# Optimization experiments

Measured on AMD Instinct MI355X. Metric: run time of the kernel, lower is better.

Reference implementation:

```python
import jax, jax.numpy as jnp
import numpy as np

NUM_HEADS = 4
BN_EPS = 1e-5


def setup_inputs() -> dict:
    key = jax.random.key(0)
    k1, k2, k3 = jax.random.split(key, 3)
    B, C, H, W = 4, 512, 64, 64
    c_attn = 256
    x = jax.random.normal(k1, (B, C, H, W), dtype=jnp.float32)
    # 1x1 convs are plain channel matmuls: weight[out, in]
    w_qkv = jax.random.normal(k2, (3 * c_attn, c_attn), dtype=jnp.float32) * (c_attn ** -0.5)
    w_proj = jax.random.normal(k3, (c_attn, c_attn), dtype=jnp.float32) * (c_attn ** -0.5)
    gamma = jnp.ones((c_attn,), dtype=jnp.float32)
    beta = jnp.zeros((c_attn,), dtype=jnp.float32)
    return {"x": x, "w_qkv": w_qkv, "w_proj": w_proj, "gamma": gamma, "beta": beta}


def reference(x, w_qkv, w_proj, gamma, beta):
    B, C, H, W = x.shape
    c_attn = w_proj.shape[0]
    head_dim = c_attn // NUM_HEADS
    scale = head_dim ** -0.5
    N = H * W

    x_attn = x[:, :c_attn].reshape(B, c_attn, N)   # [B, c_attn, N]
    x_skip = x[:, c_attn:]                          # [B, c_skip, H, W]

    # 1x1 conv qkv (no bias): [B, 3*c_attn, N]
    qkv = jnp.einsum('oc,bcn->bon', w_qkv, x_attn)
    qkv = qkv.reshape(B, 3, NUM_HEADS, head_dim, N)
    q, k, v = qkv[:, 0], qkv[:, 1], qkv[:, 2]       # each [B, h, d, N]

    # attn[b,h,i,j] = sum_d q[b,h,d,i] * k[b,h,d,j] * scale
    attn = jnp.einsum('bhdn,bhdm->bhnm', q, k) * scale
    attn = jax.nn.softmax(attn, axis=-1)

    # out[b,h,d,i] = sum_j attn[b,h,i,j] * v[b,h,d,j]
    out = jnp.einsum('bhnm,bhdm->bhdn', attn, v).reshape(B, c_attn, N)

    # 1x1 conv proj (no bias)
    out = jnp.einsum('oc,bcn->bon', w_proj, out)

    # BatchNorm2d (training mode: batch statistics over B and spatial dims)
    mean = out.mean(axis=(0, 2), keepdims=True)
    var = out.var(axis=(0, 2), keepdims=True)  # biased variance, as torch BN
    out = (out - mean) * jax.lax.rsqrt(var + BN_EPS)
    out = out * gamma[None, :, None] + beta[None, :, None]

    out = out.reshape(B, c_attn, H, W)
    return jnp.concatenate([out, x_skip], axis=1)
```

## Files before the change

kernel.cpp:

```cpp
#include <hip/hip_runtime.h>
#include <stdint.h>

typedef float          f32x4  __attribute__((ext_vector_type(4)));
typedef __bf16         bf16x8 __attribute__((ext_vector_type(8)));
typedef unsigned short u16x4  __attribute__((ext_vector_type(4)));
typedef unsigned short u16x8  __attribute__((ext_vector_type(8)));

__device__ __forceinline__ float bf2f(unsigned short u) {
    union { uint32_t i; float f; } v; v.i = ((uint32_t)u) << 16; return v.f;
}
__device__ __forceinline__ unsigned short bfc(float f) {
    return __builtin_bit_cast(unsigned short, (__bf16)f);
}
__device__ __forceinline__ f32x4 mfma16(bf16x8 a, bf16x8 b, f32x4 c) {
    return __builtin_amdgcn_mfma_f32_16x16x32_bf16(a, b, c, 0, 0, 0);
}
__device__ __forceinline__ void async16(const unsigned short* g, unsigned short* l) {
    __builtin_amdgcn_global_load_lds(
        (const __attribute__((address_space(1))) void*)g,
        (__attribute__((address_space(3))) void*)l, 16, 0, 0);
}

#define QSC 0.18033688f

__global__ __launch_bounds__(256) void qkv_gemm(
    const float* __restrict__ x, const float* __restrict__ wqkv,
    unsigned short* __restrict__ Qb, unsigned short* __restrict__ Kb,
    unsigned short* __restrict__ Vb) {
    const int mt = blockIdx.x;
    const int nt = blockIdx.y;
    const int b  = blockIdx.z;
    const int o0 = mt * 128, n0 = nt * 128;
    __shared__ __align__(16) unsigned short Wt[128 * 72];
    __shared__ __align__(16) unsigned short Xt[128 * 72];
    const int t = threadIdx.x;
    const int lane = t & 63, w = t >> 6;
    const int wr = w >> 1, wc = w & 1;
    const int l15 = lane & 15, g = lane >> 4;

    f32x4 acc[4][4];
    const f32x4 zero = {0.f, 0.f, 0.f, 0.f};
    for (int i = 0; i < 4; i++) for (int j = 0; j < 4; j++) acc[i][j] = zero;

    for (int k0 = 0; k0 < 256; k0 += 64) {
        {
            const int row = t >> 3, col = (t & 7) * 8;
            #pragma unroll
            for (int r = 0; r < 4; r++) {
                const float* p = wqkv + (size_t)(o0 + row + r * 32) * 256 + k0 + col;
                f32x4 v0 = *(const f32x4*)p;
                f32x4 v1 = *(const f32x4*)(p + 4);
                u16x8 o8 = { bfc(v0[0]), bfc(v0[1]), bfc(v0[2]), bfc(v0[3]),
                             bfc(v1[0]), bfc(v1[1]), bfc(v1[2]), bfc(v1[3]) };
                *(u16x8*)(&Wt[(row + r * 32) * 72 + col]) = o8;
            }
        }
        {
            const int cl = t >> 4, nl = (t & 15) * 8;
            #pragma unroll
            for (int r = 0; r < 4; r++) {
                const int c = k0 + cl + r * 16;
                const float* p = x + (size_t)(b * 512 + c) * 4096 + n0 + nl;
                f32x4 v0 = *(const f32x4*)p;
                f32x4 v1 = *(const f32x4*)(p + 4);
                #pragma unroll
                for (int j = 0; j < 4; j++) Xt[(nl + j) * 72 + cl + r * 16] = bfc(v0[j]);
                #pragma unroll
                for (int j = 0; j < 4; j++) Xt[(nl + 4 + j) * 72 + cl + r * 16] = bfc(v1[j]);
            }
        }
        __syncthreads();
        #pragma unroll
        for (int kk = 0; kk < 2; kk++) {
            bf16x8 af[4], bfr[4];
            #pragma unroll
            for (int i = 0; i < 4; i++)
                af[i] = *(const bf16x8*)(&Wt[(wr * 64 + i * 16 + l15) * 72 + kk * 32 + g * 8]);
            #pragma unroll
            for (int j = 0; j < 4; j++)
                bfr[j] = *(const bf16x8*)(&Xt[(wc * 64 + j * 16 + l15) * 72 + kk * 32 + g * 8]);
            #pragma unroll
            for (int i = 0; i < 4; i++)
                #pragma unroll
                for (int j = 0; j < 4; j++)
                    acc[i][j] = mfma16(af[i], bfr[j], acc[i][j]);
        }
        __syncthreads();
    }

    #pragma unroll
    for (int i = 0; i < 4; i++) {
        const int o = o0 + wr * 64 + i * 16 + g * 4;
        #pragma unroll
        for (int j = 0; j < 4; j++) {
            const int n = n0 + wc * 64 + j * 16 + l15;
            f32x4 a = acc[i][j];
            if (o < 256) {
                u16x4 pv = { bfc(a[0] * QSC), bfc(a[1] * QSC), bfc(a[2] * QSC), bfc(a[3] * QSC) };
                const int h = o >> 6, d = o & 63;
                *(u16x4*)(&Qb[(((size_t)(b * 4 + h)) * 4096 + n) * 64 + d]) = pv;
            } else if (o < 512) {
                u16x4 pv = { bfc(a[0]), bfc(a[1]), bfc(a[2]), bfc(a[3]) };
                const int oo = o - 256; const int h = oo >> 6, d = oo & 63;
                *(u16x4*)(&Kb[(((size_t)(b * 4 + h)) * 4096 + n) * 64 + d]) = pv;
            } else {
                const int oo = o - 512; const int h = oo >> 6, d = oo & 63;
                const size_t base = (((size_t)(b * 4 + h)) * 64 + d) * 4096 + n;
                Vb[base] = bfc(a[0]); Vb[base + 4096] = bfc(a[1]);
                Vb[base + 8192] = bfc(a[2]); Vb[base + 12288] = bfc(a[3]);
            }
        }
    }
}

__global__ __launch_bounds__(256, 4) void flash_attn(
    const unsigned short* __restrict__ Qb, const unsigned short* __restrict__ Kb,
    const unsigned short* __restrict__ Vb, unsigned short* __restrict__ Opart,
    float* __restrict__ ml) {
    __shared__ __align__(16) unsigned short Kt[2][64 * 64];
    __shared__ __align__(16) unsigned short Vt[2][64 * 64];

    const int flat = (blockIdx.z * 16 + blockIdx.y) * 32 + blockIdx.x;
    const int nf = (flat & 7) * 128 + (flat >> 3);
    const int z  = nf >> 9;
    const int bh = (nf >> 5) & 15;
    const int nb = nf & 31;

    const int t = threadIdx.x, lane = t & 63, w = t >> 6;
    const int l15 = lane & 15, g = lane >> 4;
    const int xo = (l15 & 7) << 3;
    const int c0 = (g * 8) ^ xo, c1 = c0 ^ 32;
    const int vq = ((((g >> 1) ^ (l15 & 7)) << 3) | ((g & 1) << 2));

    const int rb = lane >> 3;
    const int cbe = ((lane & 7) ^ rb) << 3;
    const unsigned short* kgp = Kb + ((size_t)bh * 4096 + z * 2048 + w * 8 + rb) * 64 + cbe;
    const unsigned short* vgp = Vb + ((size_t)(bh * 64 + w * 8 + rb)) * 4096 + z * 2048 + cbe;

    auto stage = [&](int buf) {
        async16(kgp,          &Kt[buf][w * 512]);
        async16(kgp + 2048,   &Kt[buf][w * 512 + 2048]);
        async16(vgp,          &Vt[buf][w * 512]);
        async16(vgp + 131072, &Vt[buf][w * 512 + 2048]);
        kgp += 4096; vgp += 64;
    };

    bf16x8 qf[2][2];
    #pragma unroll
    for (int ntl = 0; ntl < 2; ++ntl) {
        const int nq = nb * 128 + w * 32 + ntl * 16 + l15;
        const unsigned short* qp = Qb + ((size_t)bh * 4096 + nq) * 64;
        qf[ntl][0] = *(const bf16x8*)(qp + g * 8);
        qf[ntl][1] = *(const bf16x8*)(qp + 32 + g * 8);
    }

    const bf16x8 ones8 = __builtin_bit_cast(bf16x8,
        (u16x8){0x3F80, 0x3F80, 0x3F80, 0x3F80, 0x3F80, 0x3F80, 0x3F80, 0x3F80});

    f32x4 of[4][2];
    f32x4 lf[2];
    const f32x4 zero = {0.f, 0.f, 0.f, 0.f};
    #pragma unroll
    for (int dt = 0; dt < 4; ++dt) { of[dt][0] = zero; of[dt][1] = zero; }
    lf[0] = zero; lf[1] = zero;

    stage(0);
    __syncthreads();

    for (int itp = 0; itp < 16; ++itp) {
        #pragma unroll
        for (int cur = 0; cur < 2; ++cur) {
            if (itp * 2 + cur < 31) stage(cur ^ 1);

            f32x4 st[4][2];
            __builtin_amdgcn_s_setprio(1);
            #pragma unroll
            for (int mt = 0; mt < 4; ++mt) {
                const int kro = (mt * 16 + l15) * 64;
                bf16x8 ka0 = *(const bf16x8*)(&Kt[cur][kro + c0]);
                bf16x8 ka1 = *(const bf16x8*)(&Kt[cur][kro + c1]);
                st[mt][0] = mfma16(ka1, qf[0][1], mfma16(ka0, qf[0][0], zero));
                st[mt][1] = mfma16(ka1, qf[1][1], mfma16(ka0, qf[1][0], zero));
            }
            __builtin_amdgcn_s_setprio(0);

            bf16x8 pb[2][2];
            #pragma unroll
            for (int ntl = 0; ntl < 2; ++ntl) {
                u16x4 q[4];
                #pragma unroll
                for (int mt = 0; mt < 4; ++mt) {
                    q[mt] = (u16x4){
                        bfc(__builtin_amdgcn_exp2f(st[mt][ntl][0])),
                        bfc(__builtin_amdgcn_exp2f(st[mt][ntl][1])),
                        bfc(__builtin_amdgcn_exp2f(st[mt][ntl][2])),
                        bfc(__builtin_amdgcn_exp2f(st[mt][ntl][3])) };
                }
                pb[ntl][0] = __builtin_bit_cast(bf16x8,
                    __builtin_shufflevector(q[0], q[1], 0, 1, 2, 3, 4, 5, 6, 7));
                pb[ntl][1] = __builtin_bit_cast(bf16x8,
                    __builtin_shufflevector(q[2], q[3], 0, 1, 2, 3, 4, 5, 6, 7));
            }

            const unsigned short* vb = &Vt[cur][l15 * 64];
            __builtin_amdgcn_s_setprio(1);
            lf[0] = mfma16(ones8, pb[0][1], mfma16(ones8, pb[0][0], lf[0]));
            lf[1] = mfma16(ones8, pb[1][1], mfma16(ones8, pb[1][0], lf[1]));
            #pragma unroll
            for (int dt = 0; dt < 4; ++dt) {
                const unsigned short* vr = vb + dt * 1024;
                u16x4 w00 = *(const u16x4*)(vr + (vq ^ 0));
                u16x4 w01 = *(const u16x4*)(vr + (vq ^ 16));
                u16x4 w10 = *(const u16x4*)(vr + (vq ^ 32));
                u16x4 w11 = *(const u16x4*)(vr + (vq ^ 48));
                bf16x8 va0 = __builtin_bit_cast(bf16x8,
                    __builtin_shufflevector(w00, w01, 0, 1, 2, 3, 4, 5, 6, 7));
                bf16x8 va1 = __builtin_bit_cast(bf16x8,
                    __builtin_shufflevector(w10, w11, 0, 1, 2, 3, 4, 5, 6, 7));
                of[dt][0] = mfma16(va1, pb[0][1], mfma16(va0, pb[0][0], of[dt][0]));
                of[dt][1] = mfma16(va1, pb[1][1], mfma16(va0, pb[1][0], of[dt][1]));
            }
            __builtin_amdgcn_s_setprio(0);
            __syncthreads();
        }
    }

    #pragma unroll
    for (int ntl = 0; ntl < 2; ++ntl) {
        const int nq = nb * 128 + w * 32 + ntl * 16 + l15;
        const size_t obase = ((size_t)((z * 16 + bh) * 4096 + nq)) * 64;
        #pragma unroll
        for (int dt = 0; dt < 4; ++dt) {
            u16x4 pv = { bfc(of[dt][ntl][0]), bfc(of[dt][ntl][1]),
                         bfc(of[dt][ntl][2]), bfc(of[dt][ntl][3]) };
            *(u16x4*)(&Opart[obase + dt * 16 + g * 4]) = pv;
        }
        if (g == 0) ml[z * 65536 + bh * 4096 + nq] = lf[ntl][0];
    }
}

__global__ __launch_bounds__(256) void attn_merge(
    const unsigned short* __restrict__ Opart, const float* __restrict__ ml,
    unsigned short* __restrict__ att) {
    const int tid = blockIdx.x * 256 + threadIdx.x;
    const int idx = tid >> 3;
    const int dd  = (tid & 7) * 8;
    const float inv = 1.f / (ml[idx] + ml[65536 + idx]);
    u16x8 o1 = *(const u16x8*)(Opart + (size_t)idx * 64 + dd);
    u16x8 o2 = *(const u16x8*)(Opart + 4194304u + (size_t)idx * 64 + dd);
    u16x8 o;
    #pragma unroll
    for (int j = 0; j < 8; ++j) o[j] = bfc((bf2f(o1[j]) + bf2f(o2[j])) * inv);
    const int bh = idx >> 12, n = idx & 4095;
    *(u16x8*)(&att[((size_t)((bh >> 2) * 4096 + n)) * 256 + (bh & 3) * 64 + dd]) = o;
}

__global__ __launch_bounds__(256) void proj_gemm(
    const unsigned short* __restrict__ att, const float* __restrict__ wproj,
    unsigned short* __restrict__ projbf, float* __restrict__ psum) {
    const int mt = blockIdx.x;
    const int nt = blockIdx.y;
    const int b  = blockIdx.z;
    const int o0 = mt * 128, n0 = nt * 128;
    __shared__ __align__(16) unsigned short Wt[128 * 72];
    __shared__ __align__(16) unsigned short Bt[128 * 72];
    const int t = threadIdx.x;
    const int lane = t & 63, w = t >> 6;
    const int wr = w >> 1, wc = w & 1;
    const int l15 = lane & 15, g = lane >> 4;

    f32x4 acc[4][4];
    const f32x4 zero = {0.f, 0.f, 0.f, 0.f};
    for (int i = 0; i < 4; i++) for (int j = 0; j < 4; j++) acc[i][j] = zero;

    for (int k0 = 0; k0 < 256; k0 += 64) {
        const int row = t >> 3, col = (t & 7) * 8;
        #pragma unroll
        for (int r = 0; r < 4; r++) {
            const float* p = wproj + (size_t)(o0 + row + r * 32) * 256 + k0 + col;
            f32x4 v0 = *(const f32x4*)p;
            f32x4 v1 = *(const f32x4*)(p + 4);
            u16x8 o8 = { bfc(v0[0]), bfc(v0[1]), bfc(v0[2]), bfc(v0[3]),
                         bfc(v1[0]), bfc(v1[1]), bfc(v1[2]), bfc(v1[3]) };
            *(u16x8*)(&Wt[(row + r * 32) * 72 + col]) = o8;
            u16x8 a = *(const u16x8*)(att + (((size_t)b) * 4096 + n0 + row + r * 32) * 256 + k0 + col);
            *(u16x8*)(&Bt[(row + r * 32) * 72 + col]) = a;
        }
        __syncthreads();
        #pragma unroll
        for (int kk = 0; kk < 2; kk++) {
            bf16x8 af[4], bfr[4];
            #pragma unroll
            for (int i = 0; i < 4; i++)
                af[i] = *(const bf16x8*)(&Wt[(wr * 64 + i * 16 + l15) * 72 + kk * 32 + g * 8]);
            #pragma unroll
            for (int j = 0; j < 4; j++)
                bfr[j] = *(const bf16x8*)(&Bt[(wc * 64 + j * 16 + l15) * 72 + kk * 32 + g * 8]);
            #pragma unroll
            for (int i = 0; i < 4; i++)
                #pragma unroll
                for (int j = 0; j < 4; j++)
                    acc[i][j] = mfma16(af[i], bfr[j], acc[i][j]);
        }
        __syncthreads();
    }

    #pragma unroll
    for (int i = 0; i < 4; i++) {
        const int o = o0 + wr * 64 + i * 16 + g * 4;
        #pragma unroll
        for (int j = 0; j < 4; j++) {
            const int n = n0 + wc * 64 + j * 16 + l15;
            f32x4 a = acc[i][j];
            #pragma unroll
            for (int r = 0; r < 4; r++)
                projbf[((size_t)(b * 256 + o + r)) * 4096 + n] = bfc(a[r]);
        }
        f32x4 s = acc[i][0], q;
        #pragma unroll
        for (int r = 0; r < 4; ++r) q[r] = acc[i][0][r] * acc[i][0][r];
        #pragma unroll
        for (int j = 1; j < 4; ++j)
            #pragma unroll
            for (int r = 0; r < 4; ++r) {
                s[r] += acc[i][j][r];
                q[r] = fmaf(acc[i][j][r], acc[i][j][r], q[r]);
            }
        #pragma unroll
        for (int m = 1; m < 16; m <<= 1) {
            #pragma unroll
            for (int r = 0; r < 4; ++r) {
                s[r] += __shfl_xor(s[r], m, 64);
                q[r] += __shfl_xor(q[r], m, 64);
            }
        }
        if (l15 == 0) {
            const int slot = (b * 32 + nt) * 2 + wc;
            *(f32x4*)(&psum[slot * 256 + o]) = s;
            *(f32x4*)(&psum[65536 + slot * 256 + o]) = q;
        }
    }
}

__global__ __launch_bounds__(256) void bn_finalize(const float* __restrict__ psum,
                                                   float* __restrict__ stats) {
    const int o = blockIdx.x, t = threadIdx.x;
    const int lane = t & 63, w = t >> 6;
    float s = psum[t * 256 + o];
    float q = psum[65536 + t * 256 + o];
    #pragma unroll
    for (int m = 1; m < 64; m <<= 1) {
        s += __shfl_xor(s, m, 64);
        q += __shfl_xor(q, m, 64);
    }
    __shared__ float red[8];
    if (lane == 0) { red[w] = s; red[4 + w] = q; }
    __syncthreads();
    if (t == 0) {
        const float S = red[0] + red[1] + red[2] + red[3];
        const float Q = red[4] + red[5] + red[6] + red[7];
        const float mean = S * (1.f / 16384.f);
        const float var = Q * (1.f / 16384.f) - mean * mean;
        stats[o] = mean;
        stats[256 + o] = rsqrtf(var + 1e-5f);
    }
}

__global__ __launch_bounds__(256) void bn_apply(
    const unsigned short* __restrict__ projbf, const float* __restrict__ stats,
    const float* __restrict__ gamma, const float* __restrict__ beta,
    const float* __restrict__ x, float* __restrict__ out) {
    const size_t idx8 = ((size_t)blockIdx.x * 256 + threadIdx.x) * 8;
    const int n  = (int)(idx8 & 4095);
    const int ch = (int)((idx8 >> 12) & 511);
    const int b  = (int)(idx8 >> 21);
    if (ch < 256) {
        const float mean = stats[ch], rstd = stats[256 + ch];
        const float sc = gamma[ch] * rstd;
        const float sh = beta[ch] - mean * sc;
        u16x8 pv = *(const u16x8*)(projbf + (((size_t)(b * 256 + ch)) << 12) + n);
        f32x4 o0, o1;
        #pragma unroll
        for (int j = 0; j < 4; j++) { o0[j] = bf2f(pv[j]) * sc + sh; o1[j] = bf2f(pv[4 + j]) * sc + sh; }
        *(f32x4*)(out + idx8) = o0;
        *(f32x4*)(out + idx8 + 4) = o1;
    } else {
        *(f32x4*)(out + idx8)     = *(const f32x4*)(x + idx8);
        *(f32x4*)(out + idx8 + 4) = *(const f32x4*)(x + idx8 + 4);
    }
}

extern "C" void kernel_launch(void* const* d_in, const int* in_sizes, int n_in,
                              void* d_out, int out_size, void* d_ws, size_t ws_size,
                              hipStream_t stream) {
    const float* x     = (const float*)d_in[0];
    const float* wqkv  = (const float*)d_in[1];
    const float* wproj = (const float*)d_in[2];
    const float* gamma = (const float*)d_in[3];
    const float* beta  = (const float*)d_in[4];
    float* out = (float*)d_out;

    char* ws = (char*)d_ws;
    unsigned short* Qb     = (unsigned short*)(ws);
    unsigned short* Kb     = (unsigned short*)(ws + (8ull  << 20));
    unsigned short* Vb     = (unsigned short*)(ws + (16ull << 20));
    unsigned short* Opart  = (unsigned short*)(ws + (24ull << 20));
    float*          ml     = (float*)(ws + (41ull << 20));
    unsigned short* att    = (unsigned short*)(ws);
    unsigned short* projbf = (unsigned short*)(ws + (9ull  << 20));
    float*          psum   = (float*)(ws + (18ull << 20));
    float*          stats  = (float*)(ws + (18ull << 20) + (600u << 10));

    qkv_gemm   <<<dim3(6, 32, 4),  256, 0, stream>>>(x, wqkv, Qb, Kb, Vb);
    flash_attn <<<dim3(32, 16, 2), 256, 0, stream>>>(Qb, Kb, Vb, Opart, ml);
    attn_merge <<<2048,            256, 0, stream>>>(Opart, ml, att);
    proj_gemm  <<<dim3(2, 32, 4),  256, 0, stream>>>(att, wproj, projbf, psum);
    bn_finalize<<<256,             256, 0, stream>>>(psum, stats);
    bn_apply   <<<4096,            256, 0, stream>>>(projbf, stats, gamma, beta, x, out);
}
```

Before: 148.0 us.

## Double flash-attn query tile per wave and fuse split-K merge into proj GEMM

Each flash-attention wave now handles 64 query rows instead of 32, so the K/V tiles loaded into registers from LDS are reused across four query sub-tiles. The block count halves and the launch bound drops to 2 blocks per SM to make room for more registers. The separate attn_merge kernel is removed: proj_gemm now reads both split-K partial outputs and the row sums directly, normalising as it stages the B tile. This cuts LDS reads per MFMA and drops one kernel launch plus an intermediate round trip through global memory. The cost is more register pressure, lower occupancy, fewer blocks to fill the GPU, and repeated merge work in proj_gemm for each M tile.

```diff
diff --git a/kernel.cpp b/kernel.cpp
--- a/kernel.cpp
+++ b/kernel.cpp
@@ -113,18 +113,18 @@
     }
 }
 
-__global__ __launch_bounds__(256, 4) void flash_attn(
+__global__ __launch_bounds__(256, 2) void flash_attn(
     const unsigned short* __restrict__ Qb, const unsigned short* __restrict__ Kb,
     const unsigned short* __restrict__ Vb, unsigned short* __restrict__ Opart,
     float* __restrict__ ml) {
     __shared__ __align__(16) unsigned short Kt[2][64 * 64];
     __shared__ __align__(16) unsigned short Vt[2][64 * 64];
 
-    const int flat = (blockIdx.z * 16 + blockIdx.y) * 32 + blockIdx.x;
-    const int nf = (flat & 7) * 128 + (flat >> 3);
-    const int z  = nf >> 9;
-    const int bh = (nf >> 5) & 15;
-    const int nb = nf & 31;
+    const int flat = (blockIdx.z * 16 + blockIdx.y) * 16 + blockIdx.x;
+    const int nf = (flat & 7) * 64 + (flat >> 3);
+    const int z  = nf >> 8;
+    const int bh = (nf >> 4) & 15;
+    const int nb = nf & 15;
 
     const int t = threadIdx.x, lane = t & 63, w = t >> 6;
     const int l15 = lane & 15, g = lane >> 4;
@@ -145,10 +145,10 @@
         kgp += 4096; vgp += 64;
     };
 
-    bf16x8 qf[2][2];
-    #pragma unroll
-    for (int ntl = 0; ntl < 2; ++ntl) {
-        const int nq = nb * 128 + w * 32 + ntl * 16 + l15;
+    bf16x8 qf[4][2];
+    #pragma unroll
+    for (int ntl = 0; ntl < 4; ++ntl) {
+        const int nq = nb * 256 + w * 64 + ntl * 16 + l15;
         const unsigned short* qp = Qb + ((size_t)bh * 4096 + nq) * 64;
         qf[ntl][0] = *(const bf16x8*)(qp + g * 8);
         qf[ntl][1] = *(const bf16x8*)(qp + 32 + g * 8);
@@ -157,12 +157,14 @@
     const bf16x8 ones8 = __builtin_bit_cast(bf16x8,
         (u16x8){0x3F80, 0x3F80, 0x3F80, 0x3F80, 0x3F80, 0x3F80, 0x3F80, 0x3F80});
 
-    f32x4 of[4][2];
-    f32x4 lf[2];
+    f32x4 of[4][4];
+    f32x4 lf[4];
     const f32x4 zero = {0.f, 0.f, 0.f, 0.f};
     #pragma unroll
-    for (int dt = 0; dt < 4; ++dt) { of[dt][0] = zero; of[dt][1] = zero; }
-    lf[0] = zero; lf[1] = zero;
+    for (int dt = 0; dt < 4; ++dt)
+        #pragma unroll
+        for (int ntl = 0; ntl < 4; ++ntl) of[dt][ntl] = zero;
+    lf[0] = zero; lf[1] = zero; lf[2] = zero; lf[3] = zero;
 
     stage(0);
     __syncthreads();
@@ -172,62 +174,72 @@
         for (int cur = 0; cur < 2; ++cur) {
             if (itp * 2 + cur < 31) stage(cur ^ 1);
 
-            f32x4 st[4][2];
-            __builtin_amdgcn_s_setprio(1);
+            bf16x8 ka[4][2], va[4][2];
             #pragma unroll
             for (int mt = 0; mt < 4; ++mt) {
                 const int kro = (mt * 16 + l15) * 64;
-                bf16x8 ka0 = *(const bf16x8*)(&Kt[cur][kro + c0]);
-                bf16x8 ka1 = *(const bf16x8*)(&Kt[cur][kro + c1]);
-                st[mt][0] = mfma16(ka1, qf[0][1], mfma16(ka0, qf[0][0], zero));
-                st[mt][1] = mfma16(ka1, qf[1][1], mfma16(ka0, qf[1][0], zero));
-            }
-            __builtin_amdgcn_s_setprio(0);
-
-            bf16x8 pb[2][2];
-            #pragma unroll
-            for (int ntl = 0; ntl < 2; ++ntl) {
-                u16x4 q[4];
-                #pragma unroll
-                for (int mt = 0; mt < 4; ++mt) {
-                    q[mt] = (u16x4){
-                        bfc(__builtin_amdgcn_exp2f(st[mt][ntl][0])),
-                        bfc(__builtin_amdgcn_exp2f(st[mt][ntl][1])),
-                        bfc(__builtin_amdgcn_exp2f(st[mt][ntl][2])),
-                        bfc(__builtin_amdgcn_exp2f(st[mt][ntl][3])) };
-                }
-                pb[ntl][0] = __builtin_bit_cast(bf16x8,
-                    __builtin_shufflevector(q[0], q[1], 0, 1, 2, 3, 4, 5, 6, 7));
-                pb[ntl][1] = __builtin_bit_cast(bf16x8,
-                    __builtin_shufflevector(q[2], q[3], 0, 1, 2, 3, 4, 5, 6, 7));
-            }
-
-            const unsigned short* vb = &Vt[cur][l15 * 64];
-            __builtin_amdgcn_s_setprio(1);
-            lf[0] = mfma16(ones8, pb[0][1], mfma16(ones8, pb[0][0], lf[0]));
-            lf[1] = mfma16(ones8, pb[1][1], mfma16(ones8, pb[1][0], lf[1]));
+                ka[mt][0] = *(const bf16x8*)(&Kt[cur][kro + c0]);
+                ka[mt][1] = *(const bf16x8*)(&Kt[cur][kro + c1]);
+            }
             #pragma unroll
             for (int dt = 0; dt < 4; ++dt) {
-                const unsigned short* vr = vb + dt * 1024;
+                const unsigned short* vr = &Vt[cur][l15 * 64 + dt * 1024];
                 u16x4 w00 = *(const u16x4*)(vr + (vq ^ 0));
                 u16x4 w01 = *(const u16x4*)(vr + (vq ^ 16));
                 u16x4 w10 = *(const u16x4*)(vr + (vq ^ 32));
                 u16x4 w11 = *(const u16x4*)(vr + (vq ^ 48));
-                bf16x8 va0 = __builtin_bit_cast(bf16x8,
+                va[dt][0] = __builtin_bit_cast(bf16x8,
                     __builtin_shufflevector(w00, w01, 0, 1, 2, 3, 4, 5, 6, 7));
-                bf16x8 va1 = __builtin_bit_cast(bf16x8,
+                va[dt][1] = __builtin_bit_cast(bf16x8,
                     __builtin_shufflevector(w10, w11, 0, 1, 2, 3, 4, 5, 6, 7));
-                of[dt][0] = mfma16(va1, pb[0][1], mfma16(va0, pb[0][0], of[dt][0]));
-                of[dt][1] = mfma16(va1, pb[1][1], mfma16(va0, pb[1][0], of[dt][1]));
-            }
-            __builtin_amdgcn_s_setprio(0);
+            }
+
+            #pragma unroll
+            for (int ntl = 0; ntl < 4; ++ntl) {
+                f32x4 st[4];
+                __builtin_amdgcn_s_setprio(1);
+                #pragma unroll
+                for (int mt = 0; mt < 4; ++mt)
+                    st[mt] = mfma16(ka[mt][1], qf[ntl][1],
+                                    mfma16(ka[mt][0], qf[ntl][0], zero));
+                __builtin_amdgcn_s_setprio(0);
+
+                u16x4 q0 = { bfc(__builtin_amdgcn_exp2f(st[0][0])),
+                             bfc(__builtin_amdgcn_exp2f(st[0][1])),
+                             bfc(__builtin_amdgcn_exp2f(st[0][2])),
+                             bfc(__builtin_amdgcn_exp2f(st[0][3])) };
+                u16x4 q1 = { bfc(__builtin_amdgcn_exp2f(st[1][0])),
+                             bfc(__builtin_amdgcn_exp2f(st[1][1])),
+                             bfc(__builtin_amdgcn_exp2f(st[1][2])),
+                             bfc(__builtin_amdgcn_exp2f(st[1][3])) };
+                u16x4 q2 = { bfc(__builtin_amdgcn_exp2f(st[2][0])),
+                             bfc(__builtin_amdgcn_exp2f(st[2][1])),
+                             bfc(__builtin_amdgcn_exp2f(st[2][2])),
+                             bfc(__builtin_amdgcn_exp2f(st[2][3])) };
+                u16x4 q3 = { bfc(__builtin_amdgcn_exp2f(st[3][0])),
+                             bfc(__builtin_amdgcn_exp2f(st[3][1])),
+                             bfc(__builtin_amdgcn_exp2f(st[3][2])),
+                             bfc(__builtin_amdgcn_exp2f(st[3][3])) };
+                bf16x8 pb0 = __builtin_bit_cast(bf16x8,
+                    __builtin_shufflevector(q0, q1, 0, 1, 2, 3, 4, 5, 6, 7));
+                bf16x8 pb1 = __builtin_bit_cast(bf16x8,
+                    __builtin_shufflevector(q2, q3, 0, 1, 2, 3, 4, 5, 6, 7));
+
+                __builtin_amdgcn_s_setprio(1);
+                lf[ntl] = mfma16(ones8, pb1, mfma16(ones8, pb0, lf[ntl]));
+                #pragma unroll
+                for (int dt = 0; dt < 4; ++dt)
+                    of[dt][ntl] = mfma16(va[dt][1], pb1,
+                                         mfma16(va[dt][0], pb0, of[dt][ntl]));
+                __builtin_amdgcn_s_setprio(0);
+            }
             __syncthreads();
         }
     }
 
     #pragma unroll
-    for (int ntl = 0; ntl < 2; ++ntl) {
-        const int nq = nb * 128 + w * 32 + ntl * 16 + l15;
+    for (int ntl = 0; ntl < 4; ++ntl) {
+        const int nq = nb * 256 + w * 64 + ntl * 16 + l15;
         const size_t obase = ((size_t)((z * 16 + bh) * 4096 + nq)) * 64;
         #pragma unroll
         for (int dt = 0; dt < 4; ++dt) {
@@ -239,24 +251,9 @@
     }
 }
 
-__global__ __launch_bounds__(256) void attn_merge(
+__global__ __launch_bounds__(256) void proj_gemm(
     const unsigned short* __restrict__ Opart, const float* __restrict__ ml,
-    unsigned short* __restrict__ att) {
-    const int tid = blockIdx.x * 256 + threadIdx.x;
-    const int idx = tid >> 3;
-    const int dd  = (tid & 7) * 8;
-    const float inv = 1.f / (ml[idx] + ml[65536 + idx]);
-    u16x8 o1 = *(const u16x8*)(Opart + (size_t)idx * 64 + dd);
-    u16x8 o2 = *(const u16x8*)(Opart + 4194304u + (size_t)idx * 64 + dd);
-    u16x8 o;
-    #pragma unroll
-    for (int j = 0; j < 8; ++j) o[j] = bfc((bf2f(o1[j]) + bf2f(o2[j])) * inv);
-    const int bh = idx >> 12, n = idx & 4095;
-    *(u16x8*)(&att[((size_t)((bh >> 2) * 4096 + n)) * 256 + (bh & 3) * 64 + dd]) = o;
-}
-
-__global__ __launch_bounds__(256) void proj_gemm(
-    const unsigned short* __restrict__ att, const float* __restrict__ wproj,
+    const float* __restrict__ wproj,
     unsigned short* __restrict__ projbf, float* __restrict__ psum) {
     const int mt = blockIdx.x;
     const int nt = blockIdx.y;
@@ -275,6 +272,7 @@
 
     for (int k0 = 0; k0 < 256; k0 += 64) {
         const int row = t >> 3, col = (t & 7) * 8;
+        const int h = k0 >> 6;
         #pragma unroll
         for (int r = 0; r < 4; r++) {
             const float* p = wproj + (size_t)(o0 + row + r * 32) * 256 + k0 + col;
@@ -283,7 +281,14 @@
             u16x8 o8 = { bfc(v0[0]), bfc(v0[1]), bfc(v0[2]), bfc(v0[3]),
                          bfc(v1[0]), bfc(v1[1]), bfc(v1[2]), bfc(v1[3]) };
             *(u16x8*)(&Wt[(row + r * 32) * 72 + col]) = o8;
-            u16x8 a = *(const u16x8*)(att + (((size_t)b) * 4096 + n0 + row + r * 32) * 256 + k0 + col);
+            const int n = n0 + row + r * 32;
+            const int qidx = (b * 4 + h) * 4096 + n;
+            const float inv = 1.f / (ml[qidx] + ml[65536 + qidx]);
+            u16x8 m1 = *(const u16x8*)(Opart + (size_t)qidx * 64 + col);
+            u16x8 m2 = *(const u16x8*)(Opart + 4194304u + (size_t)qidx * 64 + col);
+            u16x8 a;
+            #pragma unroll
+            for (int j = 0; j < 8; ++j) a[j] = bfc((bf2f(m1[j]) + bf2f(m2[j])) * inv);
             *(u16x8*)(&Bt[(row + r * 32) * 72 + col]) = a;
         }
         __syncthreads();
@@ -406,15 +411,13 @@
     unsigned short* Vb     = (unsigned short*)(ws + (16ull << 20));
     unsigned short* Opart  = (unsigned short*)(ws + (24ull << 20));
     float*          ml     = (float*)(ws + (41ull << 20));
-    unsigned short* att    = (unsigned short*)(ws);
-    unsigned short* projbf = (unsigned short*)(ws + (9ull  << 20));
-    float*          psum   = (float*)(ws + (18ull << 20));
-    float*          stats  = (float*)(ws + (18ull << 20) + (600u << 10));
+    unsigned short* projbf = (unsigned short*)(ws);
+    float*          psum   = (float*)(ws + (9ull << 20));
+    float*          stats  = (float*)(ws + (9ull << 20) + (768u << 10));
 
     qkv_gemm   <<<dim3(6, 32, 4),  256, 0, stream>>>(x, wqkv, Qb, Kb, Vb);
-    flash_attn <<<dim3(32, 16, 2), 256, 0, stream>>>(Qb, Kb, Vb, Opart, ml);
-    attn_merge <<<2048,            256, 0, stream>>>(Opart, ml, att);
-    proj_gemm  <<<dim3(2, 32, 4),  256, 0, stream>>>(att, wproj, projbf, psum);
+    flash_attn <<<dim3(16, 16, 2), 256, 0, stream>>>(Qb, Kb, Vb, Opart, ml);
+    proj_gemm  <<<dim3(2, 32, 4),  256, 0, stream>>>(Opart, ml, wproj, projbf, psum);
     bn_finalize<<<256,             256, 0, stream>>>(psum, stats);
     bn_apply   <<<4096,            256, 0, stream>>>(projbf, stats, gamma, beta, x, out);
 }
```

New measurement: 136.1 us. -8.1%, faster.
